# Performance work log

Measured on AMD Instinct MI355X. Metric: run time of the kernel, lower is better.

The kernel has to match this reference:

```python
import jax, jax.numpy as jnp
import numpy as np

N_NODES = 50000
N_EDGES = 800000
IN_CH, HID_CH, OUT_CH = 128, 128, 40


def _glorot(key, fan_in, fan_out):
    lim = jnp.sqrt(6.0 / (fan_in + fan_out))
    return jax.random.uniform(key, (fan_in, fan_out), jnp.float32, -lim, lim)


def setup_inputs() -> dict:
    key = jax.random.key(0)
    ks = jax.random.split(key, 5)
    x = jax.random.normal(ks[0], (N_NODES, IN_CH), jnp.float32)
    edge_index = jax.random.randint(ks[1], (2, N_EDGES), 0, N_NODES, dtype=jnp.int32)
    return {
        "x": x,
        "edge_index": edge_index,
        "W1": _glorot(ks[2], IN_CH, HID_CH),
        "b1": jnp.zeros((HID_CH,), jnp.float32),
        "W2": _glorot(ks[3], HID_CH, HID_CH),
        "b2": jnp.zeros((HID_CH,), jnp.float32),
        "W3": _glorot(ks[4], HID_CH, OUT_CH),
        "b3": jnp.zeros((OUT_CH,), jnp.float32),
    }


def reference(x, edge_index, W1, b1, W2, b2, W3, b3):
    # Dropout is inference-mode identity (training=False). GCNConv (PyG default):
    # add self-loops, symmetric normalization D^-1/2 A_hat D^-1/2, linear + bias.
    n = x.shape[0]
    loop = jnp.arange(n, dtype=edge_index.dtype)
    src = jnp.concatenate([edge_index[0], loop])  # message sources
    dst = jnp.concatenate([edge_index[1], loop])  # aggregation targets
    deg = jax.ops.segment_sum(jnp.ones_like(src, dtype=x.dtype), dst, num_segments=n)
    dinv = jnp.where(deg > 0, deg ** -0.5, 0.0)
    norm = dinv[src] * dinv[dst]  # [E+N], identical across layers

    def conv(h, W, b):
        h = h @ W                                   # [N, F_out]
        msg = h[src] * norm[:, None]                # gather + scale: [E+N, F_out]
        return jax.ops.segment_sum(msg, dst, num_segments=n) + b

    h = jax.nn.relu(conv(x, W1, b1))
    h = jax.nn.relu(conv(h, W2, b2))
    h = conv(h, W3, b3)
    return jax.nn.log_softmax(h, axis=1)
```

## Files before the change

kernel.cpp:

```cpp
#include <hip/hip_runtime.h>
#include <math.h>


typedef short s8v __attribute__((ext_vector_type(8)));
typedef float f4v __attribute__((ext_vector_type(4)));

#define CSR_CAP 64

__device__ inline unsigned short f2b(float f) {
  unsigned int u = __float_as_uint(f);
  return (unsigned short)((u + 0x7fffu + ((u >> 16) & 1u)) >> 16);
}
__device__ inline float b2f(unsigned short b) {
  return __uint_as_float(((unsigned int)b) << 16);
}
__device__ inline f4v mfma16(s8v a, s8v b, f4v c) {
  return __builtin_amdgcn_mfma_f32_16x16x32_bf16(a, b, c, 0, 0, 0);
}

__device__ inline void pack_w_elem(const float* __restrict__ W,
                                   short* __restrict__ Wp, int FOUT_real,
                                   int NCT, int idx) {
  const int j = idx & 7;
  const int lane = (idx >> 3) & 63;
  const int fct = idx >> 9;
  const int ks = fct / NCT, ct = fct - ks * NCT;
  const int k = ks * 32 + (lane >> 4) * 8 + j;
  const int c = ct * 16 + (lane & 15);
  const float v = (c < FOUT_real) ? W[k * FOUT_real + c] : 0.f;
  Wp[idx] = (short)f2b(v);
}

__global__ __launch_bounds__(256) void k_soup(
    const float* __restrict__ x, const float* __restrict__ W1,
    short* __restrict__ Tb1, int nRowTiles, int gemmNB,
    const int* __restrict__ src, const int* __restrict__ dst,
    int* __restrict__ cnt, int* __restrict__ col, int e, float inv8n,
    int fillNB, const float* __restrict__ W2, short* __restrict__ Wp2,
    const float* __restrict__ W3, short* __restrict__ Wp3) {
  __shared__ short Ws[4 * 8 * 64 * 8];
  const int bid = blockIdx.x;
  const int tid = threadIdx.x;

  if (bid < gemmNB) {
    const float4* w4 = (const float4*)W1;
    for (int it = 0; it < 16; ++it) {
      const int lin4 = it * 256 + tid;
      const int k = lin4 >> 5;
      const float4 v = w4[lin4];
      const int cb = (lin4 & 31) * 4;
      const int ks = k >> 5, kr = k & 31;
      const int laneBase = (kr >> 3) << 4;
      const int j = kr & 7;
      const float fv[4] = {v.x, v.y, v.z, v.w};
#pragma unroll
      for (int q = 0; q < 4; ++q) {
        const int c = cb + q;
        Ws[((ks * 8 + (c >> 4)) * 64 + (laneBase | (c & 15))) * 8 + j] =
            (short)f2b(fv[q]);
      }
    }
    __syncthreads();
    const int wid = tid >> 6, lane = tid & 63;
    const int rowTile = bid * 4 + wid;
    if (rowTile >= nRowTiles) return;
    const int row0 = rowTile * 16;
    const int arow = row0 + (lane & 15);
    const int kcol = (lane >> 4) * 8;
    f4v acc[8];
#pragma unroll
    for (int ct = 0; ct < 8; ++ct) acc[ct] = (f4v)(0.f);
    const float* ap = x + (size_t)arow * 128 + kcol;
#pragma unroll
    for (int ks = 0; ks < 4; ++ks) {
      const float4 a0 = *(const float4*)(ap + ks * 32);
      const float4 a1 = *(const float4*)(ap + ks * 32 + 4);
      s8v af;
      af[0] = (short)f2b(a0.x); af[1] = (short)f2b(a0.y);
      af[2] = (short)f2b(a0.z); af[3] = (short)f2b(a0.w);
      af[4] = (short)f2b(a1.x); af[5] = (short)f2b(a1.y);
      af[6] = (short)f2b(a1.z); af[7] = (short)f2b(a1.w);
#pragma unroll
      for (int ct = 0; ct < 8; ++ct) {
        const s8v bf = *(const s8v*)(Ws + ((ks * 8 + ct) * 64 + lane) * 8);
        acc[ct] = mfma16(af, bf, acc[ct]);
      }
    }
    const int crow0 = row0 + (lane >> 4) * 4;
    const int ccol = lane & 15;
#pragma unroll
    for (int r = 0; r < 4; ++r) {
      short* orow = Tb1 + (size_t)(crow0 + r) * 128 + ccol;
#pragma unroll
      for (int ct = 0; ct < 8; ++ct) orow[ct * 16] = (short)f2b(acc[ct][r]);
    }
  } else if (bid < gemmNB + fillNB) {
    const int fb = bid - gemmNB;
    const int bin = fb & 7;
    const int scanB = fb >> 3;
    const int stride = (fillNB >> 3) * 256;
    for (int i = scanB * 256 + tid; i < e; i += stride) {
      const int d = dst[i];
      int b = (int)((float)d * inv8n);
      b = b > 7 ? 7 : b;
      if (b == bin) {
        const int idx = atomicAdd(&cnt[d], 1);
        col[(size_t)d * CSR_CAP + idx] = src[i];
      }
    }
  } else {
    int pb = bid - gemmNB - fillNB;
    if (pb < 64) {
      pack_w_elem(W2, Wp2, 128, 8, pb * 256 + tid);
    } else {
      const int idx = (pb - 64) * 256 + tid;
      if (idx < 128 * 48) pack_w_elem(W3, Wp3, 40, 3, idx);
    }
  }
}

template <int FIN, int FOUT>
__global__ __launch_bounds__(256) void k_gemm_mfma(const short* __restrict__ Hb,
                                                   const short* __restrict__ Wp,
                                                   short* __restrict__ Tb,
                                                   int nRowTiles) {
  constexpr int NCT = FOUT / 16;
  constexpr int NKS = FIN / 32;
  __shared__ short Ws[NKS * NCT * 64 * 8];
  for (int i = threadIdx.x; i < NKS * NCT * 64; i += 256)
    ((s8v*)Ws)[i] = ((const s8v*)Wp)[i];
  __syncthreads();
  const int wid = threadIdx.x >> 6;
  const int lane = threadIdx.x & 63;
  const int rowTile = blockIdx.x * 4 + wid;
  if (rowTile >= nRowTiles) return;
  const int row0 = rowTile * 16;
  const int arow = row0 + (lane & 15);
  const int kcol = (lane >> 4) * 8;
  f4v acc[NCT];
#pragma unroll
  for (int ct = 0; ct < NCT; ++ct) acc[ct] = (f4v)(0.f);
  const short* aptr = Hb + (size_t)arow * FIN + kcol;
#pragma unroll
  for (int ks = 0; ks < NKS; ++ks) {
    const s8v afrag = *(const s8v*)(aptr + ks * 32);
#pragma unroll
    for (int ct = 0; ct < NCT; ++ct) {
      const s8v bfrag = *(const s8v*)(Ws + ((ks * NCT + ct) * 64 + lane) * 8);
      acc[ct] = mfma16(afrag, bfrag, acc[ct]);
    }
  }
  const int crow0 = row0 + (lane >> 4) * 4;
  const int ccol = lane & 15;
#pragma unroll
  for (int r = 0; r < 4; ++r) {
    short* orow = Tb + (size_t)(crow0 + r) * FOUT + ccol;
#pragma unroll
    for (int ct = 0; ct < NCT; ++ct)
      orow[ct * 16] = (short)f2b(acc[ct][r]);
  }
}

template <int F, bool RELU>
__global__ __launch_bounds__(256) void k_agg_scale(const short* __restrict__ Tb,
                                                   const int* __restrict__ cnt,
                                                   const int* __restrict__ col,
                                                   const float* __restrict__ bias,
                                                   short* __restrict__ O, int n) {
  constexpr int TPN = F / 8;
  const int gtid = blockIdx.x * 256 + threadIdx.x;
  const int node = gtid / TPN;
  const int c8 = gtid - node * TPN;
  if (node >= n) return;
  const int c0 = c8 * 8;
  const int cn = cnt[node];
  const float dn = rsqrtf((float)(cn + 1));
  float acc[8];
  {
    const s8v v = *(const s8v*)(Tb + (size_t)node * F + c0);
#pragma unroll
    for (int j = 0; j < 8; ++j) acc[j] = dn * b2f((unsigned short)v[j]);
  }
  const int beg = node * CSR_CAP;
  const int end = beg + cn;
  for (int k = beg; k < end; ++k) {
    const int s = col[k];
    const float ds = rsqrtf((float)(cnt[s] + 1));
    const s8v v = *(const s8v*)(Tb + (size_t)s * F + c0);
#pragma unroll
    for (int j = 0; j < 8; ++j) acc[j] += ds * b2f((unsigned short)v[j]);
  }
  s8v o;
#pragma unroll
  for (int j = 0; j < 8; ++j) {
    float r = acc[j] * dn + bias[c0 + j];
    if (RELU) r = fmaxf(r, 0.f);
    o[j] = (short)f2b(r);
  }
  *(s8v*)(O + (size_t)node * F + c0) = o;
}

__global__ __launch_bounds__(256) void k_agg3_lsm(const short* __restrict__ Tb,
                                                  const int* __restrict__ cnt,
                                                  const int* __restrict__ col,
                                                  const float* __restrict__ bias,
                                                  float* __restrict__ out, int n) {
  const int gtid = blockIdx.x * 256 + threadIdx.x;
  const int node = gtid >> 3;
  const int c8 = gtid & 7;
  if (node >= n) return;
  const int c0 = c8 * 8;
  const bool valid = c8 < 5;
  const int cn = cnt[node];
  const float dn = rsqrtf((float)(cn + 1));
  float acc[8];
#pragma unroll
  for (int j = 0; j < 8; ++j) acc[j] = 0.f;
  if (valid) {
    const s8v v = *(const s8v*)(Tb + (size_t)node * 48 + c0);
#pragma unroll
    for (int j = 0; j < 8; ++j) acc[j] = dn * b2f((unsigned short)v[j]);
  }
  const int beg = node * CSR_CAP;
  const int end = beg + cn;
  for (int k = beg; k < end; ++k) {
    const int s = col[k];
    if (valid) {
      const float ds = rsqrtf((float)(cnt[s] + 1));
      const s8v v = *(const s8v*)(Tb + (size_t)s * 48 + c0);
#pragma unroll
      for (int j = 0; j < 8; ++j) acc[j] += ds * b2f((unsigned short)v[j]);
    }
  }
  float r[8];
  float m = -INFINITY;
#pragma unroll
  for (int j = 0; j < 8; ++j) {
    r[j] = valid ? (acc[j] * dn + bias[c0 + j]) : -INFINITY;
    m = fmaxf(m, r[j]);
  }
#pragma unroll
  for (int w = 1; w < 8; w <<= 1) m = fmaxf(m, __shfl_xor(m, w, 64));
  float s = 0.f;
#pragma unroll
  for (int j = 0; j < 8; ++j) s += expf(r[j] - m);
#pragma unroll
  for (int w = 1; w < 8; w <<= 1) s += __shfl_xor(s, w, 64);
  const float ls = logf(s);
  if (valid) {
    float* op = out + (size_t)node * 40 + c0;
    *(float4*)op = make_float4(r[0] - m - ls, r[1] - m - ls, r[2] - m - ls,
                               r[3] - m - ls);
    *(float4*)(op + 4) = make_float4(r[4] - m - ls, r[5] - m - ls,
                                     r[6] - m - ls, r[7] - m - ls);
  }
}

extern "C" void kernel_launch(void* const* d_in, const int* in_sizes, int n_in,
                              void* d_out, int out_size, void* d_ws,
                              size_t ws_size, hipStream_t stream) {
  const float* x  = (const float*)d_in[0];
  const int*   ei = (const int*)d_in[1];
  const float* W1 = (const float*)d_in[2];
  const float* b1 = (const float*)d_in[3];
  const float* W2 = (const float*)d_in[4];
  const float* b2 = (const float*)d_in[5];
  const float* W3 = (const float*)d_in[6];
  const float* b3 = (const float*)d_in[7];
  float* out = (float*)d_out;

  const int n = in_sizes[0] / 128;
  const int e = in_sizes[1] / 2;
  const int* src = ei;
  const int* dst = ei + e;

  char* ws = (char*)d_ws;
  size_t off = 0;
  auto carve = [&](size_t bytes) -> void* {
    void* p = ws + off;
    off = (off + bytes + 255) & ~(size_t)255;
    return p;
  };
  int*   cnt = (int*)carve((size_t)n * 4);
  int*   col = (int*)carve((size_t)n * CSR_CAP * 4);
  short* A   = (short*)carve((size_t)n * 128 * 2);
  short* B   = (short*)carve((size_t)n * 128 * 2);
  short* Wp2 = (short*)carve(128 * 128 * 2);
  short* Wp3 = (short*)carve(128 * 48 * 2);

  const int nRowTiles = (n + 15) / 16;
  const int gemmNB = (nRowTiles + 3) / 4;
  const int fillNB = 2048;
  const int soupNB = gemmNB + fillNB + 64 + 24;

  hipMemsetAsync(cnt, 0, (size_t)n * 4, stream);
  k_soup<<<soupNB, 256, 0, stream>>>(x, W1, B, nRowTiles, gemmNB, src, dst,
                                     cnt, col, e, 8.0f / (float)n, fillNB,
                                     W2, Wp2, W3, Wp3);

  const int agg128Grid = ((size_t)n * 16 + 255) / 256;
  const int agg8Grid   = ((size_t)n * 8 + 255) / 256;

  k_agg_scale<128, true><<<agg128Grid, 256, 0, stream>>>(B, cnt, col, b1, A, n);
  k_gemm_mfma<128, 128><<<gemmNB, 256, 0, stream>>>(A, Wp2, B, nRowTiles);
  k_agg_scale<128, true><<<agg128Grid, 256, 0, stream>>>(B, cnt, col, b2, A, n);
  k_gemm_mfma<128, 48><<<gemmNB, 256, 0, stream>>>(A, Wp3, B, nRowTiles);
  k_agg3_lsm<<<agg8Grid, 256, 0, stream>>>(B, cnt, col, b3, out, n);
}
```

Measured before the change: 258.3 us.

## Fuse aggregation with next-layer GEMM and shrink CSR indices to 16-bit

Merges each aggregation+bias+ReLU pass with the following MFMA GEMM into a single kernel. The aggregated 32-row tile is staged in swizzled LDS and multiplied by weights read directly from global memory. This removes two launches and the round trip of the intermediate activation through HBM. CSR column indices are also stored as u16 to halve index traffic, but node ids go up to 50000, which exceeds the signed short range only if read as signed. As u16 they fit under 65535, so this holds only while N stays below 65536.

New measurement: 240.5 us. 6.9% less time.

```diff
diff --git a/kernel.cpp b/kernel.cpp
--- a/kernel.cpp
+++ b/kernel.cpp
@@ -4,6 +4,7 @@
 
 typedef short s8v __attribute__((ext_vector_type(8)));
 typedef float f4v __attribute__((ext_vector_type(4)));
+typedef unsigned short u16;
 
 #define CSR_CAP 64
 
@@ -35,7 +36,7 @@
     const float* __restrict__ x, const float* __restrict__ W1,
     short* __restrict__ Tb1, int nRowTiles, int gemmNB,
     const int* __restrict__ src, const int* __restrict__ dst,
-    int* __restrict__ cnt, int* __restrict__ col, int e, float inv8n,
+    int* __restrict__ cnt, u16* __restrict__ col, int e, float inv8n,
     int fillNB, const float* __restrict__ W2, short* __restrict__ Wp2,
     const float* __restrict__ W3, short* __restrict__ Wp3) {
   __shared__ short Ws[4 * 8 * 64 * 8];
@@ -105,7 +106,7 @@
       b = b > 7 ? 7 : b;
       if (b == bin) {
         const int idx = atomicAdd(&cnt[d], 1);
-        col[(size_t)d * CSR_CAP + idx] = src[i];
+        col[(size_t)d * CSR_CAP + idx] = (u16)src[i];
       }
     }
   } else {
@@ -119,90 +120,95 @@
   }
 }
 
-template <int FIN, int FOUT>
-__global__ __launch_bounds__(256) void k_gemm_mfma(const short* __restrict__ Hb,
-                                                   const short* __restrict__ Wp,
-                                                   short* __restrict__ Tb,
-                                                   int nRowTiles) {
+template <int FOUT>
+__global__ __launch_bounds__(256) void k_aggemm(const short* __restrict__ Tb,
+                                                const int* __restrict__ cnt,
+                                                const u16* __restrict__ col,
+                                                const float* __restrict__ bias,
+                                                const short* __restrict__ Wp,
+                                                short* __restrict__ Tout, int n) {
+  __shared__ short Ht[32 * 128];
+  const int tid = threadIdx.x;
+  const int base = blockIdx.x * 32;
+
+#pragma unroll
+  for (int pass = 0; pass < 2; ++pass) {
+    const int nl = pass * 16 + (tid >> 4);
+    const int node = base + nl;
+    const int c8 = tid & 15;
+    const int c0 = c8 * 8;
+    float r[8];
+#pragma unroll
+    for (int j = 0; j < 8; ++j) r[j] = 0.f;
+    if (node < n) {
+      const int cn = cnt[node];
+      const float dn = rsqrtf((float)(cn + 1));
+      float acc[8];
+      {
+        const s8v v = *(const s8v*)(Tb + (size_t)node * 128 + c0);
+#pragma unroll
+        for (int j = 0; j < 8; ++j) acc[j] = dn * b2f((unsigned short)v[j]);
+      }
+      const u16* cp = col + (size_t)node * CSR_CAP;
+      for (int k = 0; k < cn; ++k) {
+        const int s = cp[k];
+        const float ds = rsqrtf((float)(cnt[s] + 1));
+        const s8v v = *(const s8v*)(Tb + (size_t)s * 128 + c0);
+#pragma unroll
+        for (int j = 0; j < 8; ++j) acc[j] += ds * b2f((unsigned short)v[j]);
+      }
+#pragma unroll
+      for (int j = 0; j < 8; ++j)
+        r[j] = fmaxf(acc[j] * dn + bias[c0 + j], 0.f);
+    }
+    s8v o;
+#pragma unroll
+    for (int j = 0; j < 8; ++j) o[j] = (short)f2b(r[j]);
+    *(s8v*)((char*)Ht + nl * 256 + ((c0 * 2) ^ ((nl & 7) << 4))) = o;
+  }
+  __syncthreads();
+
   constexpr int NCT = FOUT / 16;
-  constexpr int NKS = FIN / 32;
-  __shared__ short Ws[NKS * NCT * 64 * 8];
-  for (int i = threadIdx.x; i < NKS * NCT * 64; i += 256)
-    ((s8v*)Ws)[i] = ((const s8v*)Wp)[i];
-  __syncthreads();
-  const int wid = threadIdx.x >> 6;
-  const int lane = threadIdx.x & 63;
-  const int rowTile = blockIdx.x * 4 + wid;
-  if (rowTile >= nRowTiles) return;
-  const int row0 = rowTile * 16;
-  const int arow = row0 + (lane & 15);
-  const int kcol = (lane >> 4) * 8;
-  f4v acc[NCT];
-#pragma unroll
-  for (int ct = 0; ct < NCT; ++ct) acc[ct] = (f4v)(0.f);
-  const short* aptr = Hb + (size_t)arow * FIN + kcol;
-#pragma unroll
-  for (int ks = 0; ks < NKS; ++ks) {
-    const s8v afrag = *(const s8v*)(aptr + ks * 32);
-#pragma unroll
-    for (int ct = 0; ct < NCT; ++ct) {
-      const s8v bfrag = *(const s8v*)(Ws + ((ks * NCT + ct) * 64 + lane) * 8);
-      acc[ct] = mfma16(afrag, bfrag, acc[ct]);
-    }
-  }
-  const int crow0 = row0 + (lane >> 4) * 4;
-  const int ccol = lane & 15;
-#pragma unroll
-  for (int r = 0; r < 4; ++r) {
-    short* orow = Tb + (size_t)(crow0 + r) * FOUT + ccol;
-#pragma unroll
-    for (int ct = 0; ct < NCT; ++ct)
-      orow[ct * 16] = (short)f2b(acc[ct][r]);
-  }
-}
-
-template <int F, bool RELU>
-__global__ __launch_bounds__(256) void k_agg_scale(const short* __restrict__ Tb,
-                                                   const int* __restrict__ cnt,
-                                                   const int* __restrict__ col,
-                                                   const float* __restrict__ bias,
-                                                   short* __restrict__ O, int n) {
-  constexpr int TPN = F / 8;
-  const int gtid = blockIdx.x * 256 + threadIdx.x;
-  const int node = gtid / TPN;
-  const int c8 = gtid - node * TPN;
-  if (node >= n) return;
-  const int c0 = c8 * 8;
-  const int cn = cnt[node];
-  const float dn = rsqrtf((float)(cn + 1));
-  float acc[8];
-  {
-    const s8v v = *(const s8v*)(Tb + (size_t)node * F + c0);
-#pragma unroll
-    for (int j = 0; j < 8; ++j) acc[j] = dn * b2f((unsigned short)v[j]);
-  }
-  const int beg = node * CSR_CAP;
-  const int end = beg + cn;
-  for (int k = beg; k < end; ++k) {
-    const int s = col[k];
-    const float ds = rsqrtf((float)(cnt[s] + 1));
-    const s8v v = *(const s8v*)(Tb + (size_t)s * F + c0);
-#pragma unroll
-    for (int j = 0; j < 8; ++j) acc[j] += ds * b2f((unsigned short)v[j]);
-  }
-  s8v o;
-#pragma unroll
-  for (int j = 0; j < 8; ++j) {
-    float r = acc[j] * dn + bias[c0 + j];
-    if (RELU) r = fmaxf(r, 0.f);
-    o[j] = (short)f2b(r);
-  }
-  *(s8v*)(O + (size_t)node * F + c0) = o;
+  const int wid = tid >> 6, lane = tid & 63;
+  const int tile = wid >> 1;
+  int ct0, nct;
+  if (FOUT == 128) { ct0 = (wid & 1) * 4; nct = 4; }
+  else { ct0 = 0; nct = (wid & 1) ? 0 : NCT; }
+  if (nct > 0) {
+    f4v acc[4];
+#pragma unroll
+    for (int j = 0; j < 4; ++j) acc[j] = (f4v)(0.f);
+    const int lrow = tile * 16 + (lane & 15);
+    const int kbase = (lane >> 4) * 8;
+#pragma unroll
+    for (int ks = 0; ks < 4; ++ks) {
+      const int kcol = kbase + ks * 32;
+      const s8v af = *(const s8v*)((const char*)Ht + lrow * 256 +
+                                   ((kcol * 2) ^ ((lrow & 7) << 4)));
+#pragma unroll
+      for (int j = 0; j < 4; ++j) {
+        if (j < nct) {
+          const s8v bf =
+              *(const s8v*)(Wp + ((ks * NCT + ct0 + j) * 64 + lane) * 8);
+          acc[j] = mfma16(af, bf, acc[j]);
+        }
+      }
+    }
+    const int crow0 = base + tile * 16 + (lane >> 4) * 4;
+    const int ccol = lane & 15;
+#pragma unroll
+    for (int r = 0; r < 4; ++r) {
+      short* orow = Tout + (size_t)(crow0 + r) * FOUT + ccol;
+#pragma unroll
+      for (int j = 0; j < 4; ++j)
+        if (j < nct) orow[(ct0 + j) * 16] = (short)f2b(acc[j][r]);
+    }
+  }
 }
 
 __global__ __launch_bounds__(256) void k_agg3_lsm(const short* __restrict__ Tb,
                                                   const int* __restrict__ cnt,
-                                                  const int* __restrict__ col,
+                                                  const u16* __restrict__ col,
                                                   const float* __restrict__ bias,
                                                   float* __restrict__ out, int n) {
   const int gtid = blockIdx.x * 256 + threadIdx.x;
@@ -221,10 +227,9 @@
 #pragma unroll
     for (int j = 0; j < 8; ++j) acc[j] = dn * b2f((unsigned short)v[j]);
   }
-  const int beg = node * CSR_CAP;
-  const int end = beg + cn;
-  for (int k = beg; k < end; ++k) {
-    const int s = col[k];
+  const u16* cp = col + (size_t)node * CSR_CAP;
+  for (int k = 0; k < cn; ++k) {
+    const int s = cp[k];
     if (valid) {
       const float ds = rsqrtf((float)(cnt[s] + 1));
       const s8v v = *(const s8v*)(Tb + (size_t)s * 48 + c0);
@@ -281,10 +286,12 @@
     off = (off + bytes + 255) & ~(size_t)255;
     return p;
   };
+  const int nb32 = (n + 31) / 32;
+  const size_t rows_pad = (size_t)nb32 * 32;
   int*   cnt = (int*)carve((size_t)n * 4);
-  int*   col = (int*)carve((size_t)n * CSR_CAP * 4);
-  short* A   = (short*)carve((size_t)n * 128 * 2);
-  short* B   = (short*)carve((size_t)n * 128 * 2);
+  u16*   col = (u16*)carve((size_t)n * CSR_CAP * 2);
+  short* A   = (short*)carve(rows_pad * 128 * 2);
+  short* B   = (short*)carve(rows_pad * 128 * 2);
   short* Wp2 = (short*)carve(128 * 128 * 2);
   short* Wp3 = (short*)carve(128 * 48 * 2);
 
@@ -297,13 +304,8 @@
   k_soup<<<soupNB, 256, 0, stream>>>(x, W1, B, nRowTiles, gemmNB, src, dst,
                                      cnt, col, e, 8.0f / (float)n, fillNB,
                                      W2, Wp2, W3, Wp3);
-
-  const int agg128Grid = ((size_t)n * 16 + 255) / 256;
-  const int agg8Grid   = ((size_t)n * 8 + 255) / 256;
-
-  k_agg_scale<128, true><<<agg128Grid, 256, 0, stream>>>(B, cnt, col, b1, A, n);
-  k_gemm_mfma<128, 128><<<gemmNB, 256, 0, stream>>>(A, Wp2, B, nRowTiles);
-  k_agg_scale<128, true><<<agg128Grid, 256, 0, stream>>>(B, cnt, col, b2, A, n);
-  k_gemm_mfma<128, 48><<<gemmNB, 256, 0, stream>>>(A, Wp3, B, nRowTiles);
-  k_agg3_lsm<<<agg8Grid, 256, 0, stream>>>(B, cnt, col, b3, out, n);
-}
+  k_aggemm<128><<<nb32, 256, 0, stream>>>(B, cnt, col, b1, Wp2, A, n);
+  k_aggemm<48><<<nb32, 256, 0, stream>>>(A, cnt, col, b2, Wp3, B, n);
+  k_agg3_lsm<<<((size_t)n * 8 + 255) / 256, 256, 0, stream>>>(B, cnt, col, b3,
+                                                              out, n);
+}
```
